# Optimization experiments

Hardware: AMD Instinct MI355X
Metric: run time of the kernel (lower is better)

## Reference

```python
import jax, jax.numpy as jnp
import numpy as np

H, W = 256, 256
L = 1024
R = 4
B = 64
EPS = 1e-4
FF = (H + W) * R * 4


def setup_inputs() -> dict:
    key = jax.random.key(0)
    ks = jax.random.split(key, 8)
    x = jax.random.normal(ks[0], (B, L), dtype=jnp.float32)
    # Linear weights (torch Linear: out = x @ W.T), kaiming-uniform-ish init
    lim = 1.0 / np.sqrt(L)
    W_t = jax.random.uniform(ks[1], (FF, L), minval=-lim, maxval=lim, dtype=jnp.float32)
    W_g = jax.random.uniform(ks[2], (FF, L), minval=-lim, maxval=lim, dtype=jnp.float32)
    # weights_static: [2, H, W, 2]
    k_lim = np.sqrt(6.0 / (H * W))
    ws0 = jax.random.uniform(ks[3], (1, H, W, 2), minval=-k_lim, maxval=k_lim, dtype=jnp.float32)
    ws1_re = jax.random.uniform(ks[4], (1, H, W, 1), minval=EPS - 1.0, maxval=1.0 - EPS, dtype=jnp.float32)
    ws1_im = jax.random.uniform(ks[5], (1, H, W, 1), minval=-EPS, maxval=EPS, dtype=jnp.float32)
    weights_static = jnp.concatenate([ws0, jnp.concatenate([ws1_re, ws1_im], axis=-1)], axis=0)
    x_lim = np.sqrt(6.0 / (H + W))
    weights_mod = jax.random.uniform(ks[6], (4, H, W), minval=-x_lim, maxval=x_lim, dtype=jnp.float32)
    c_lim = 1.0 / np.sqrt(R)
    kc1, kc2 = jax.random.split(ks[7])
    conv_w = jax.random.uniform(kc1, (R, R), minval=-c_lim, maxval=c_lim, dtype=jnp.float32)  # [out_ch, in_ch] for 1x1 conv
    conv_b = jax.random.uniform(kc2, (R,), minval=-c_lim, maxval=c_lim, dtype=jnp.float32)
    return {"x": x, "W_t": W_t, "W_g": W_g, "weights_static": weights_static,
            "weights_mod": weights_mod, "conv_w": conv_w, "conv_b": conv_b}


def reference(x, W_t, W_g, weights_static, weights_mod, conv_w, conv_b):
    b = x.shape[0]
    xt = x @ W_t.T                                  # [B, FF]
    xg = x @ W_g.T
    xg = xg * jax.nn.sigmoid(xg)                    # SiLU-style gate
    mod = xt * xg
    mod = mod.reshape(b, 4, -1)
    mod = mod / jnp.sqrt(jnp.mean(jnp.abs(mod), axis=-1, keepdims=True) + EPS)
    mod = mod.reshape(b, 4, R, H + W)
    a_part = mod[..., :H]                           # [B,4,R,H]
    b_part = mod[..., H:]                           # [B,4,R,W]
    outer = jnp.einsum('bkri,bkrj->bkrij', a_part, b_part)  # [B,4,R,H,W]
    # 1x1 conv (R->R) followed by sum over output channels collapses to a
    # single contraction with column-summed weights + summed bias (same math).
    w_eff = conv_w.sum(axis=0)                      # [R]
    b_eff = conv_b.sum()
    mod = jnp.einsum('bkrij,r->bkij', outer, w_eff) + b_eff  # [B,4,H,W]
    mod = weights_mod[None] * mod
    A0 = weights_static[0]                          # [H,W,2]
    A1 = weights_static[1]                          # [H,W,2]
    Bc = jnp.moveaxis(mod[:, 0:2], 1, -1)           # [B,H,W,2]
    re = A1[..., 0] * Bc[..., 0] - A1[..., 1] * Bc[..., 1]
    im = A1[..., 0] * Bc[..., 1] - A1[..., 1] * Bc[..., 0]
    mag = jnp.sqrt(re * re + im * im + EPS)         # [B,H,W]
    mag = jnp.sqrt(jnp.mean(mag, axis=(-1, -2)) + EPS)  # [B]
    inv = 1.0 / mag[:, None, None]
    mw_re = A0[..., 0] + re * inv                   # [B,H,W]
    mw_im = A0[..., 1] + im * inv
    proj = jnp.moveaxis(mod[:, 2:4], 1, -1)         # [B,H,W,2]
    den = jnp.sqrt(proj[..., 0] ** 2 + proj[..., 1] ** 2 + EPS)
    theta_cos = proj[..., 0] / den
    theta_sin = proj[..., 1] / den
    return mw_re * theta_cos + mw_im * theta_sin    # [B,H,W]
```

## Files before the change

### kernel.cpp

```cpp
#include <hip/hip_runtime.h>

typedef __bf16 bf16x8 __attribute__((ext_vector_type(8)));
typedef float floatx4 __attribute__((ext_vector_type(4)));

__device__ inline void cvt8_hl(const float* __restrict__ p, bf16x8& h, bf16x8& l){
  float4 v0 = *reinterpret_cast<const float4*>(p);
  float4 v1 = *reinterpret_cast<const float4*>(p + 4);
  float v[8] = {v0.x, v0.y, v0.z, v0.w, v1.x, v1.y, v1.z, v1.w};
  #pragma unroll
  for (int i = 0; i < 8; ++i) {
    __bf16 hi = (__bf16)v[i];
    h[i] = hi;
    l[i] = (__bf16)(v[i] - (float)hi);
  }
}

__global__ __launch_bounds__(256) void k1_gemm(
    const float* __restrict__ x,
    const float* __restrict__ Wt,
    const float* __restrict__ Wg,
    float* __restrict__ mod)
{
  __shared__ float red[3][32][64];
  const int tid  = threadIdx.x;
  const int wave = tid >> 6, lane = tid & 63;
  const int quad = lane >> 4, r16 = lane & 15;
  const int ff = blockIdx.x * 16 + r16;
  const int kb = wave * 256 + quad * 8;

  floatx4 accT[4], accG[4];
  #pragma unroll
  for (int m = 0; m < 4; ++m) { accT[m] = (floatx4)0.0f; accG[m] = (floatx4)0.0f; }

  const float* wt = Wt + ff * 1024 + kb;
  const float* wg = Wg + ff * 1024 + kb;
  const float* xp = x  + r16 * 1024 + kb;

  #pragma unroll
  for (int it = 0; it < 8; ++it) {
    const int ko = it * 32;
    bf16x8 bth, btl, bgh, bgl;
    cvt8_hl(wt + ko, bth, btl);
    cvt8_hl(wg + ko, bgh, bgl);
    #pragma unroll
    for (int mt = 0; mt < 4; ++mt) {
      bf16x8 ah, al;
      cvt8_hl(xp + mt * 16384 + ko, ah, al);
      accT[mt] = __builtin_amdgcn_mfma_f32_16x16x32_bf16(ah, bth, accT[mt], 0, 0, 0);
      accT[mt] = __builtin_amdgcn_mfma_f32_16x16x32_bf16(ah, btl, accT[mt], 0, 0, 0);
      accT[mt] = __builtin_amdgcn_mfma_f32_16x16x32_bf16(al, bth, accT[mt], 0, 0, 0);
      accG[mt] = __builtin_amdgcn_mfma_f32_16x16x32_bf16(ah, bgh, accG[mt], 0, 0, 0);
      accG[mt] = __builtin_amdgcn_mfma_f32_16x16x32_bf16(ah, bgl, accG[mt], 0, 0, 0);
      accG[mt] = __builtin_amdgcn_mfma_f32_16x16x32_bf16(al, bgh, accG[mt], 0, 0, 0);
    }
  }

  if (wave != 0) {
    #pragma unroll
    for (int mt = 0; mt < 4; ++mt)
      #pragma unroll
      for (int r = 0; r < 4; ++r) {
        red[wave - 1][mt * 4 + r][lane]      = accT[mt][r];
        red[wave - 1][16 + mt * 4 + r][lane] = accG[mt][r];
      }
  }
  __syncthreads();
  if (wave == 0) {
    #pragma unroll
    for (int mt = 0; mt < 4; ++mt) {
      #pragma unroll
      for (int r = 0; r < 4; ++r) {
        float t = accT[mt][r] + red[0][mt * 4 + r][lane]
                              + red[1][mt * 4 + r][lane]
                              + red[2][mt * 4 + r][lane];
        float g = accG[mt][r] + red[0][16 + mt * 4 + r][lane]
                              + red[1][16 + mt * 4 + r][lane]
                              + red[2][16 + mt * 4 + r][lane];
        float sig = 1.0f / (1.0f + __expf(-g));
        int b = mt * 16 + quad * 4 + r;
        mod[b * 8192 + ff] = t * g * sig;
      }
    }
  }
}

__global__ __launch_bounds__(256) void k1b_scale(const float* __restrict__ mod,
                                                 const float* __restrict__ wmod,
                                                 const float* __restrict__ wstat,
                                                 float* __restrict__ s)
{
  const int row = blockIdx.x;
  const int tid = threadIdx.x;
  const float* p = mod + row * 2048;

  const int g = blockIdx.x * 256 + tid;
  const float4 wv = reinterpret_cast<const float4*>(wmod)[g];
  const float4 sv = reinterpret_cast<const float4*>(wstat)[g];
  float keep = wv.x + wv.y + wv.z + wv.w + sv.x + sv.y + sv.z + sv.w;
  asm volatile("" :: "v"(keep));

  float sum = 0.0f;
  #pragma unroll
  for (int q = 0; q < 8; ++q) sum += fabsf(p[q * 256 + tid]);
  #pragma unroll
  for (int o = 1; o < 64; o <<= 1) sum += __shfl_xor(sum, o, 64);
  __shared__ float ls[4];
  if ((tid & 63) == 0) ls[tid >> 6] = sum;
  __syncthreads();
  if (tid == 0) {
    float t = ls[0] + ls[1] + ls[2] + ls[3];
    s[row] = rsqrtf(t * (1.0f / 2048.0f) + 1e-4f);
  }
}

__global__ __launch_bounds__(256) void k2_mag(
    const float* __restrict__ mod, const float* __restrict__ s,
    const float* __restrict__ wstat,
    const float* __restrict__ wmod,
    const float* __restrict__ cw,
    const float* __restrict__ cb,
    float* __restrict__ partial)
{
  const int b = blockIdx.x, jc = blockIdx.y;
  const int tid = threadIdx.x;
  __shared__ __align__(16) float a_l[256 * 8];

  float weff[4]; float beff = 0.0f;
  #pragma unroll
  for (int r = 0; r < 4; ++r) {
    weff[r] = cw[r] + cw[4 + r] + cw[8 + r] + cw[12 + r];
    beff += cb[r];
  }
  const float s0 = s[b * 4 + 0], s1 = s[b * 4 + 1];
  const float* mb = mod + b * 8192;

  #pragma unroll
  for (int p = 0; p < 8; ++p) {
    int k = p >> 2, r = p & 3;
    float sc = (k ? s1 : s0) * weff[r];
    a_l[tid * 8 + p] = mb[k * 2048 + r * 512 + tid] * sc;
  }
  const int j = jc * 32 + (tid & 31);
  float bp[8];
  #pragma unroll
  for (int p = 0; p < 8; ++p) {
    int k = p >> 2, r = p & 3;
    bp[p] = mb[k * 2048 + r * 512 + 256 + j] * (k ? s1 : s0);
  }
  __syncthreads();

  const int ioff = tid >> 5;
  float acc = 0.0f;
  #pragma unroll 8
  for (int it = 0; it < 32; ++it) {
    const int i = it * 8 + ioff;
    const float4 av0 = *reinterpret_cast<const float4*>(&a_l[i * 8]);
    const float4 av1 = *reinterpret_cast<const float4*>(&a_l[i * 8 + 4]);
    float d0 = av0.x * bp[0] + av0.y * bp[1] + av0.z * bp[2] + av0.w * bp[3];
    float d1 = av1.x * bp[4] + av1.y * bp[5] + av1.z * bp[6] + av1.w * bp[7];
    const int ij = i * 256 + j;
    float m0 = wmod[ij] * (d0 + beff);
    float m1 = wmod[65536 + ij] * (d1 + beff);
    float2 a1 = *reinterpret_cast<const float2*>(wstat + 131072 + ij * 2);
    float re = a1.x * m0 - a1.y * m1;
    float im = a1.x * m1 - a1.y * m0;
    acc += sqrtf(re * re + im * im + 1e-4f);
  }
  #pragma unroll
  for (int o = 1; o < 64; o <<= 1) acc += __shfl_xor(acc, o, 64);
  __shared__ float wsum[4];
  if ((tid & 63) == 0) wsum[tid >> 6] = acc;
  __syncthreads();
  if (tid == 0) partial[b * 8 + jc] = wsum[0] + wsum[1] + wsum[2] + wsum[3];
}

__global__ __launch_bounds__(256) void k4_out(
    const float* __restrict__ mod, const float* __restrict__ s,
    const float* __restrict__ wstat,
    const float* __restrict__ wmod,
    const float* __restrict__ cw,
    const float* __restrict__ cb,
    const float* __restrict__ partial,
    float* __restrict__ out)
{
  const int b = blockIdx.x, ibase = blockIdx.y * 32;
  const int tid = threadIdx.x;
  __shared__ __align__(16) float a_l[32 * 16];

  float weff[4]; float beff = 0.0f;
  #pragma unroll
  for (int r = 0; r < 4; ++r) {
    weff[r] = cw[r] + cw[4 + r] + cw[8 + r] + cw[12 + r];
    beff += cb[r];
  }
  float sk[4];
  #pragma unroll
  for (int k = 0; k < 4; ++k) sk[k] = s[b * 4 + k];
  const float* mb = mod + b * 8192;

  float tot = 0.0f;
  #pragma unroll
  for (int t = 0; t < 8; ++t) tot += partial[b * 8 + t];
  const float inv = rsqrtf(tot * (1.0f / 65536.0f) + 1e-4f);

  #pragma unroll
  for (int p = 0; p < 2; ++p) {
    int idx = p * 256 + tid;
    int il = idx & 31, kr = idx >> 5;
    int k = kr >> 2, r = kr & 3;
    a_l[il * 16 + kr] = mb[k * 2048 + r * 512 + ibase + il] * (sk[k] * weff[r]);
  }
  const int j = (tid & 127) * 2;
  const int ioff = tid >> 7;
  float bp0[16], bp1[16];
  #pragma unroll
  for (int kr = 0; kr < 16; ++kr) {
    int k = kr >> 2, r = kr & 3;
    float2 v = *reinterpret_cast<const float2*>(mb + k * 2048 + r * 512 + 256 + j);
    bp0[kr] = v.x * sk[k]; bp1[kr] = v.y * sk[k];
  }
  __syncthreads();

  #pragma unroll 4
  for (int it = 0; it < 16; ++it) {
    const int il = it * 2 + ioff;
    const int i = ibase + il;
    const float4 a0 = *reinterpret_cast<const float4*>(&a_l[il * 16]);
    const float4 a1 = *reinterpret_cast<const float4*>(&a_l[il * 16 + 4]);
    const float4 a2 = *reinterpret_cast<const float4*>(&a_l[il * 16 + 8]);
    const float4 a3 = *reinterpret_cast<const float4*>(&a_l[il * 16 + 12]);
    const int ij = i * 256 + j;
    const float2 wm0 = *reinterpret_cast<const float2*>(wmod + ij);
    const float2 wm1 = *reinterpret_cast<const float2*>(wmod + 65536 + ij);
    const float2 wm2 = *reinterpret_cast<const float2*>(wmod + 131072 + ij);
    const float2 wm3 = *reinterpret_cast<const float2*>(wmod + 196608 + ij);
    const float4 A0v = *reinterpret_cast<const float4*>(wstat + ij * 2);
    const float4 A1v = *reinterpret_cast<const float4*>(wstat + 131072 + ij * 2);
    float outv[2];
    #pragma unroll
    for (int e = 0; e < 2; ++e) {
      const float* bp = e ? bp1 : bp0;
      float d0 = a0.x * bp[0] + a0.y * bp[1] + a0.z * bp[2] + a0.w * bp[3];
      float d1 = a1.x * bp[4] + a1.y * bp[5] + a1.z * bp[6] + a1.w * bp[7];
      float d2 = a2.x * bp[8] + a2.y * bp[9] + a2.z * bp[10] + a2.w * bp[11];
      float d3 = a3.x * bp[12] + a3.y * bp[13] + a3.z * bp[14] + a3.w * bp[15];
      float m0 = (e ? wm0.y : wm0.x) * (d0 + beff);
      float m1 = (e ? wm1.y : wm1.x) * (d1 + beff);
      float m2 = (e ? wm2.y : wm2.x) * (d2 + beff);
      float m3 = (e ? wm3.y : wm3.x) * (d3 + beff);
      float A0r = e ? A0v.z : A0v.x;
      float A0i = e ? A0v.w : A0v.y;
      float A1r = e ? A1v.z : A1v.x;
      float A1i = e ? A1v.w : A1v.y;
      float re = A1r * m0 - A1i * m1;
      float im = A1r * m1 - A1i * m0;
      float mwre = A0r + re * inv;
      float mwim = A0i + im * inv;
      float rd = rsqrtf(m2 * m2 + m3 * m3 + 1e-4f);
      outv[e] = (mwre * m2 + mwim * m3) * rd;
    }
    *reinterpret_cast<float2*>(out + b * 65536 + ij) = make_float2(outv[0], outv[1]);
  }
}

extern "C" void kernel_launch(void* const* d_in, const int* in_sizes, int n_in,
                              void* d_out, int out_size, void* d_ws, size_t ws_size,
                              hipStream_t stream) {
  const float* x     = (const float*)d_in[0];
  const float* Wt    = (const float*)d_in[1];
  const float* Wg    = (const float*)d_in[2];
  const float* wstat = (const float*)d_in[3];
  const float* wmod  = (const float*)d_in[4];
  const float* cw    = (const float*)d_in[5];
  const float* cb    = (const float*)d_in[6];

  float* mod     = (float*)d_ws;
  float* sbuf    = mod + 524288;
  float* partial = sbuf + 256;

  k1_gemm  <<<512, 256, 0, stream>>>(x, Wt, Wg, mod);
  k1b_scale<<<256, 256, 0, stream>>>(mod, wmod, wstat, sbuf);
  k2_mag   <<<dim3(64, 8), 256, 0, stream>>>(mod, sbuf, wstat, wmod, cw, cb, partial);
  k4_out   <<<dim3(64, 8), 256, 0, stream>>>(mod, sbuf, wstat, wmod, cw, cb, partial,
                                             (float*)d_out);
}
```

Measured before the change: 149.8 us.

## Stage GEMM weights through double-buffered LDS and split batch across waves

The gate/value GEMM kernel now partitions work by batch rows per wave instead of splitting K across waves, which removes the cross-wave shared-memory reduction. Weight tiles for W_t and W_g are staged into a double-buffered, XOR-swizzled LDS buffer with direct global-to-LDS loads, so each wave reads them from LDS while the next chunk is prefetched. It adds a barrier per K chunk and assumes the LDS swizzle and load layout line up. Each weight element is also now converted to hi/lo bf16 by all four waves instead of once.

```diff
diff --git a/kernel.cpp b/kernel.cpp
--- a/kernel.cpp
+++ b/kernel.cpp
@@ -13,6 +13,22 @@
     h[i] = hi;
     l[i] = (__bf16)(v[i] - (float)hi);
   }
+}
+
+__device__ inline void cvt8v(float4 v0, float4 v1, bf16x8& h, bf16x8& l){
+  float v[8] = {v0.x, v0.y, v0.z, v0.w, v1.x, v1.y, v1.z, v1.w};
+  #pragma unroll
+  for (int i = 0; i < 8; ++i) {
+    __bf16 hi = (__bf16)v[i];
+    h[i] = hi;
+    l[i] = (__bf16)(v[i] - (float)hi);
+  }
+}
+
+__device__ inline void gload_lds16(const float* g, float* l){
+  __builtin_amdgcn_global_load_lds(
+      (const __attribute__((address_space(1))) unsigned int*)g,
+      (__attribute__((address_space(3))) unsigned int*)l, 16, 0, 0);
 }
 
 __global__ __launch_bounds__(256) void k1_gemm(
@@ -21,66 +37,76 @@
     const float* __restrict__ Wg,
     float* __restrict__ mod)
 {
-  __shared__ float red[3][32][64];
+  __shared__ __align__(16) float wlds[2][2][16 * 128];
   const int tid  = threadIdx.x;
   const int wave = tid >> 6, lane = tid & 63;
   const int quad = lane >> 4, r16 = lane & 15;
-  const int ff = blockIdx.x * 16 + r16;
-  const int kb = wave * 256 + quad * 8;
-
-  floatx4 accT[4], accG[4];
-  #pragma unroll
-  for (int m = 0; m < 4; ++m) { accT[m] = (floatx4)0.0f; accG[m] = (floatx4)0.0f; }
-
-  const float* wt = Wt + ff * 1024 + kb;
-  const float* wg = Wg + ff * 1024 + kb;
-  const float* xp = x  + r16 * 1024 + kb;
-
-  #pragma unroll
-  for (int it = 0; it < 8; ++it) {
-    const int ko = it * 32;
-    bf16x8 bth, btl, bgh, bgl;
-    cvt8_hl(wt + ko, bth, btl);
-    cvt8_hl(wg + ko, bgh, bgl);
+  const int ffbase = blockIdx.x * 16;
+
+  int soff[4], sdst[4];
+  #pragma unroll
+  for (int u = 0; u < 4; ++u) {
+    int t = wave * 4 + u;
+    int mat = t >> 3, rowpair = (t & 7) * 2;
+    int row = rowpair + (lane >> 5);
+    int cb  = (lane & 31) * 16;
+    soff[u] = (ffbase + row) * 1024 + ((cb ^ ((row & 7) << 4)) >> 2);
+    sdst[u] = mat * 2048 + rowpair * 128;
+    soff[u] = mat ? soff[u] : soff[u];
+  }
+  const int m0 = (wave * 4 + 0) >> 3, m1 = (wave * 4 + 1) >> 3;
+  const int m2 = (wave * 4 + 2) >> 3, m3 = (wave * 4 + 3) >> 3;
+
+  auto STAGE = [&](int buf, int kc) {
+    gload_lds16((m0 ? Wg : Wt) + soff[0] + kc, &wlds[buf][0][0] + sdst[0]);
+    gload_lds16((m1 ? Wg : Wt) + soff[1] + kc, &wlds[buf][0][0] + sdst[1]);
+    gload_lds16((m2 ? Wg : Wt) + soff[2] + kc, &wlds[buf][0][0] + sdst[2]);
+    gload_lds16((m3 ? Wg : Wt) + soff[3] + kc, &wlds[buf][0][0] + sdst[3]);
+  };
+
+  const float* xp = x + (wave * 16 + r16) * 1024;
+  const int rowb = r16 * 512;
+  const int xr   = (r16 & 7) << 4;
+
+  floatx4 accT = (floatx4)0.0f, accG = (floatx4)0.0f;
+
+  STAGE(0, 0);
+  __syncthreads();
+
+  #pragma unroll
+  for (int c = 0; c < 8; ++c) {
+    const int kc = c * 128;
+    if (c < 7) STAGE((c + 1) & 1, kc + 128);
+    const char* tT = (const char*)&wlds[c & 1][0][0];
+    const char* tG = (const char*)&wlds[c & 1][1][0];
     #pragma unroll
-    for (int mt = 0; mt < 4; ++mt) {
-      bf16x8 ah, al;
-      cvt8_hl(xp + mt * 16384 + ko, ah, al);
-      accT[mt] = __builtin_amdgcn_mfma_f32_16x16x32_bf16(ah, bth, accT[mt], 0, 0, 0);
-      accT[mt] = __builtin_amdgcn_mfma_f32_16x16x32_bf16(ah, btl, accT[mt], 0, 0, 0);
-      accT[mt] = __builtin_amdgcn_mfma_f32_16x16x32_bf16(al, bth, accT[mt], 0, 0, 0);
-      accG[mt] = __builtin_amdgcn_mfma_f32_16x16x32_bf16(ah, bgh, accG[mt], 0, 0, 0);
-      accG[mt] = __builtin_amdgcn_mfma_f32_16x16x32_bf16(ah, bgl, accG[mt], 0, 0, 0);
-      accG[mt] = __builtin_amdgcn_mfma_f32_16x16x32_bf16(al, bgh, accG[mt], 0, 0, 0);
+    for (int kk = 0; kk < 4; ++kk) {
+      const int cb  = kk * 128 + quad * 32;
+      const int aLo = rowb + (cb ^ xr);
+      const int aHi = rowb + ((cb + 16) ^ xr);
+      bf16x8 ah, al, bth, btl, bgh, bgl;
+      cvt8_hl(xp + kc + kk * 32 + quad * 8, ah, al);
+      cvt8v(*reinterpret_cast<const float4*>(tT + aLo),
+            *reinterpret_cast<const float4*>(tT + aHi), bth, btl);
+      cvt8v(*reinterpret_cast<const float4*>(tG + aLo),
+            *reinterpret_cast<const float4*>(tG + aHi), bgh, bgl);
+      accT = __builtin_amdgcn_mfma_f32_16x16x32_bf16(ah, bth, accT, 0, 0, 0);
+      accT = __builtin_amdgcn_mfma_f32_16x16x32_bf16(ah, btl, accT, 0, 0, 0);
+      accT = __builtin_amdgcn_mfma_f32_16x16x32_bf16(al, bth, accT, 0, 0, 0);
+      accG = __builtin_amdgcn_mfma_f32_16x16x32_bf16(ah, bgh, accG, 0, 0, 0);
+      accG = __builtin_amdgcn_mfma_f32_16x16x32_bf16(ah, bgl, accG, 0, 0, 0);
+      accG = __builtin_amdgcn_mfma_f32_16x16x32_bf16(al, bgh, accG, 0, 0, 0);
     }
-  }
-
-  if (wave != 0) {
-    #pragma unroll
-    for (int mt = 0; mt < 4; ++mt)
-      #pragma unroll
-      for (int r = 0; r < 4; ++r) {
-        red[wave - 1][mt * 4 + r][lane]      = accT[mt][r];
-        red[wave - 1][16 + mt * 4 + r][lane] = accG[mt][r];
-      }
-  }
-  __syncthreads();
-  if (wave == 0) {
-    #pragma unroll
-    for (int mt = 0; mt < 4; ++mt) {
-      #pragma unroll
-      for (int r = 0; r < 4; ++r) {
-        float t = accT[mt][r] + red[0][mt * 4 + r][lane]
-                              + red[1][mt * 4 + r][lane]
-                              + red[2][mt * 4 + r][lane];
-        float g = accG[mt][r] + red[0][16 + mt * 4 + r][lane]
-                              + red[1][16 + mt * 4 + r][lane]
-                              + red[2][16 + mt * 4 + r][lane];
-        float sig = 1.0f / (1.0f + __expf(-g));
-        int b = mt * 16 + quad * 4 + r;
-        mod[b * 8192 + ff] = t * g * sig;
-      }
-    }
+    __syncthreads();
+  }
+
+  #pragma unroll
+  for (int r = 0; r < 4; ++r) {
+    float t = accT[r];
+    float g = accG[r];
+    float sig = 1.0f / (1.0f + __expf(-g));
+    const int b = wave * 16 + quad * 4 + r;
+    mod[b * 8192 + ffbase + r16] = t * g * sig;
   }
 }
 
```

Result: slower. 154.0 us (+2.8%).
